# Optimization experiments

Hardware: AMD Instinct MI355X
Metric: run time of the kernel (lower is better)

Reference implementation:

```python
import jax, jax.numpy as jnp
import numpy as np
from jax import lax

C = 192       # filter_channels
L = 3         # n_layers
K = 3         # kernel_size
NB = 10       # num_bins
TB = 5.0      # tail_bound
HALF = 1      # in_channels // 2


def setup_inputs() -> dict:
    key = jax.random.key(0)
    ks = jax.random.split(key, 8)
    s = lambda i, shape: jax.random.normal(ks[i], shape, jnp.float32) * 0.05
    return {
        "x": jax.random.normal(ks[0], (16, 2, 8192), jnp.float32),
        "x_mask": jnp.ones((16, 1, 8192), jnp.float32),
        "w_pre": s(1, (C, HALF)), "b_pre": jnp.zeros((C,), jnp.float32),
        "sep_w": s(2, (L, K, 1, C)), "sep_b": jnp.zeros((L, C), jnp.float32),
        "pw_w": s(3, (L, C, C)), "pw_b": jnp.zeros((L, C), jnp.float32),
        "n1_g": jnp.ones((L, C), jnp.float32), "n1_b": jnp.zeros((L, C), jnp.float32),
        "n2_g": jnp.ones((L, C), jnp.float32), "n2_b": jnp.zeros((L, C), jnp.float32),
        "w_proj": s(4, (HALF * (3 * NB - 1), C)),
        "b_proj": jnp.zeros((HALF * (3 * NB - 1),), jnp.float32),
    }


def _layernorm_c(x, g, b, eps=1e-5):
    # normalize over channel axis (axis=1) of [b, c, t]
    m = jnp.mean(x, axis=1, keepdims=True)
    v = jnp.var(x, axis=1, keepdims=True)
    return (x - m) * lax.rsqrt(v + eps) * g[:, None] + b[:, None]


def _rq_spline(x, uw, uh, ud, tail_bound=TB, mw=1e-3, mh=1e-3, md=1e-3):
    """Unconstrained rational-quadratic spline with linear tails (forward)."""
    nb = uw.shape[-1]
    inside = (x >= -tail_bound) & (x <= tail_bound)
    const = float(np.log(np.exp(1.0 - md) - 1.0))
    ud = jnp.pad(ud, [(0, 0)] * (ud.ndim - 1) + [(1, 1)], constant_values=const)

    widths = jax.nn.softmax(uw, axis=-1)
    widths = mw + (1.0 - mw * nb) * widths
    cw = jnp.pad(jnp.cumsum(widths, -1), [(0, 0)] * (widths.ndim - 1) + [(1, 0)])
    cw = -tail_bound + 2.0 * tail_bound * cw
    cw = cw.at[..., 0].set(-tail_bound).at[..., -1].set(tail_bound)
    w = cw[..., 1:] - cw[..., :-1]

    heights = jax.nn.softmax(uh, axis=-1)
    heights = mh + (1.0 - mh * nb) * heights
    ch = jnp.pad(jnp.cumsum(heights, -1), [(0, 0)] * (heights.ndim - 1) + [(1, 0)])
    ch = -tail_bound + 2.0 * tail_bound * ch
    ch = ch.at[..., 0].set(-tail_bound).at[..., -1].set(tail_bound)
    hgt = ch[..., 1:] - ch[..., :-1]

    d = md + jax.nn.softplus(ud)  # [..., nb+1]

    xi = jnp.clip(x, -tail_bound, tail_bound)
    # searchsorted-style bin lookup
    idx = jnp.clip(jnp.sum((xi[..., None] >= cw).astype(jnp.int32), -1) - 1, 0, nb - 1)
    take = lambda p: jnp.take_along_axis(p, idx[..., None], axis=-1)[..., 0]

    in_cw, in_w = take(cw), take(w)
    in_ch, in_h = take(ch), take(hgt)
    in_d, d_p = take(d), take(d[..., 1:])
    delta = in_h / in_w

    th = (xi - in_cw) / in_w
    th1 = th * (1.0 - th)
    num = in_h * (delta * th * th + in_d * th1)
    den = delta + (in_d + d_p - 2.0 * delta) * th1
    y = in_ch + num / den
    dnum = delta * delta * (d_p * th * th + 2.0 * delta * th1 + in_d * (1.0 - th) ** 2)
    lad = jnp.log(dnum) - 2.0 * jnp.log(den)

    y = jnp.where(inside, y, x)
    lad = jnp.where(inside, lad, jnp.zeros_like(lad))
    return y, lad


def reference(x, x_mask, w_pre, b_pre, sep_w, sep_b, pw_w, pw_b,
              n1_g, n1_b, n2_g, n2_b, w_proj, b_proj):
    x0, x1 = x[:, :HALF], x[:, HALF:]

    # pre: 1x1 conv
    h = jnp.einsum('bct,fc->bft', x0, w_pre) + b_pre[:, None]

    # DDSConv: depthwise dilated conv + 1x1 + LayerNorm + GELU, residual
    for i in range(L):
        y = lax.conv_general_dilated(
            h * x_mask, sep_w[i], window_strides=(1,), padding='SAME',
            rhs_dilation=(K ** i,),
            dimension_numbers=('NCH', 'HIO', 'NCH'),
            feature_group_count=C) + sep_b[i][:, None]
        y = jax.nn.gelu(_layernorm_c(y, n1_g[i], n1_b[i]), approximate=False)
        y = jnp.einsum('bct,oc->bot', y, pw_w[i]) + pw_b[i][:, None]
        y = jax.nn.gelu(_layernorm_c(y, n2_g[i], n2_b[i]), approximate=False)
        h = h + y
    h = h * x_mask

    # proj: 1x1 conv to spline params
    h = (jnp.einsum('bct,oc->bot', h, w_proj) + b_proj[:, None]) * x_mask

    b, c, t = x0.shape
    h = h.reshape(b, c, 3 * NB - 1, t).transpose(0, 1, 3, 2)  # [b, c, t, 3*NB-1]
    scale = 1.0 / np.sqrt(C).astype(np.float32)
    uw = h[..., :NB] * scale
    uh = h[..., NB:2 * NB] * scale
    ud = h[..., 2 * NB:]

    y1, lad = _rq_spline(x1, uw, uh, ud)
    out = jnp.concatenate([x0, y1], axis=1) * x_mask
    logdet = jnp.sum(lad * x_mask, axis=(1, 2))
    return out, logdet
```

## Files before the change

### kernel.cpp

```cpp
#include <hip/hip_runtime.h>

#define CC    192
#define EXT   76
#define LDC   216
#define NTH   512
#define NW    8
#define HALO  13
#define INTR  50
#define TT    8192
#define BATCH 16
#define NTILES 164
#define NPROJ 29

#define WQ1_ELEMS (3*6*12*512)
#define WQ2_ELEMS (6*2*512)

typedef __bf16 bf16x8 __attribute__((ext_vector_type(8)));
typedef __bf16 bf16x4 __attribute__((ext_vector_type(4)));
typedef float  f32x4  __attribute__((ext_vector_type(4)));

__device__ __forceinline__ float gelu_fast(float v) {
    float vv = v * v;
    float u2 = v * fmaf(0.0713548162f, vv, 1.5957691216f);
    float t  = __expf(u2);
    float r  = __builtin_amdgcn_rcpf(t + 1.0f);
    return v - v * r;
}
__device__ __forceinline__ float softplus_f(float v) {
    float e = __expf(-fabsf(v));
    return fmaxf(v, 0.0f) + __logf(1.0f + e);
}

__global__ __launch_bounds__(256) void prepack_kernel(
    const float* __restrict__ pw_w, const float* __restrict__ w_proj,
    __bf16* __restrict__ wq, __bf16* __restrict__ wq2) {
    int idx = blockIdx.x * 256 + threadIdx.x;
    if (idx < WQ1_ELEMS) {
        int e    = idx & 7;
        int lane = (idx >> 3) & 63;
        int r    = idx >> 9;
        int mt   = r % 12;
        int ks   = (r / 12) % 6;
        int li   = r / 72;
        int o = 16 * mt + (lane & 15);
        int c = 32 * ks + 8 * (lane >> 4) + e;
        wq[idx] = (__bf16)pw_w[((size_t)li * CC + o) * CC + c];
    } else if (idx < WQ1_ELEMS + WQ2_ELEMS) {
        int i2   = idx - WQ1_ELEMS;
        int e    = i2 & 7;
        int lane = (i2 >> 3) & 63;
        int r    = i2 >> 9;
        int mt   = r % 2;
        int ks   = r / 2;
        int row  = 16 * mt + (lane & 15);
        int c    = 32 * ks + 8 * (lane >> 4) + e;
        wq2[i2] = (row < NPROJ) ? (__bf16)w_proj[(size_t)row * CC + c] : (__bf16)0.0f;
    }
}

__global__ __launch_bounds__(NTH, 4) void convflow_kernel(
    const float* __restrict__ x, const float* __restrict__ xmask,
    const float* __restrict__ w_pre, const float* __restrict__ b_pre,
    const float* __restrict__ sep_w, const float* __restrict__ sep_b,
    const __bf16* __restrict__ wq, const __bf16* __restrict__ wq2,
    const float* __restrict__ pw_b,
    const float* __restrict__ n1_g, const float* __restrict__ n1_b,
    const float* __restrict__ n2_g, const float* __restrict__ n2_b,
    const float* __restrict__ b_proj,
    float* __restrict__ out, float* __restrict__ logdet)
{
    extern __shared__ char smemraw[];
    __bf16* __restrict__ sh_t = (__bf16*)smemraw;
    __bf16* __restrict__ syt  = sh_t + 80 * LDC;
    float*  __restrict__ sproj = (float*)syt;
    float*  __restrict__ fbase = (float*)(syt + 80 * LDC);
    float*  __restrict__ spb = fbase;
    float*  __restrict__ sg2 = fbase + 192;
    float*  __restrict__ sb2 = fbase + 384;
    float*  __restrict__ sx0 = fbase + 576;
    float*  __restrict__ sx1 = fbase + 656;
    float*  __restrict__ smk = fbase + 736;

    const int tid  = threadIdx.x;
    const int lane = tid & 63;
    const int wav  = tid >> 6;
    const int b    = blockIdx.x / NTILES;
    const int tile = blockIdx.x - b * NTILES;
    const int t0   = tile * INTR - HALO;

    for (int j = tid; j < 80; j += NTH) {
        int t = t0 + j;
        bool ok = (j < EXT) && (t >= 0) && (t < TT);
        sx0[j] = ok ? x[b*2*TT + t]      : 0.0f;
        sx1[j] = ok ? x[b*2*TT + TT + t] : 0.0f;
        smk[j] = ok ? xmask[b*TT + t]    : 0.0f;
    }
    for (int e = tid; e < 80*LDC/2; e += NTH) ((float*)syt)[e] = 0.0f;
    for (int e = tid; e < 4*LDC/2;  e += NTH) ((float*)(sh_t + 76*LDC))[e] = 0.0f;
    __syncthreads();

    for (int e = tid; e < CC*EXT; e += NTH) {
        int c = e % CC;
        int j = e / CC;
        sh_t[j*LDC + c] = (__bf16)(sx0[j] * w_pre[c] + b_pre[c]);
    }
    for (int q = tid; q < INTR; q += NTH) {
        int t = t0 + HALO + q;
        if (t < TT) out[b*2*TT + t] = sx0[HALO+q] * smk[HALO+q];
    }
    __syncthreads();

    const int cA = lane, cB = lane + 64, cD = lane + 128;
    const int g   = lane >> 4;
    const int c15 = lane & 15;

    #pragma unroll
    for (int li = 0; li < 3; ++li) {
        constexpr int DILA[3] = {1, 3, 9};
        constexpr int JLOA[3] = {1, 4, 13};
        const int dil = DILA[li];
        const int jlo = JLOA[li], jhi = EXT - JLOA[li];

        for (int i = tid; i < CC; i += NTH) {
            spb[i] = pw_b[li*CC + i];
            sg2[i] = n2_g[li*CC + i];
            sb2[i] = n2_b[li*CC + i];
        }

        {
            float k0a = sep_w[(li*3+0)*CC + cA], k1a = sep_w[(li*3+1)*CC + cA], k2a = sep_w[(li*3+2)*CC + cA];
            float k0b = sep_w[(li*3+0)*CC + cB], k1b = sep_w[(li*3+1)*CC + cB], k2b = sep_w[(li*3+2)*CC + cB];
            float k0d = sep_w[(li*3+0)*CC + cD], k1d = sep_w[(li*3+1)*CC + cD], k2d = sep_w[(li*3+2)*CC + cD];
            float cba = sep_b[li*CC + cA], cbb = sep_b[li*CC + cB], cbd = sep_b[li*CC + cD];
            float g1a = n1_g[li*CC + cA], g1b = n1_g[li*CC + cB], g1d = n1_g[li*CC + cD];
            float b1a = n1_b[li*CC + cA], b1b = n1_b[li*CC + cB], b1d = n1_b[li*CC + cD];
            for (int j = jlo + wav; j < jhi; j += NW) {
                float m0 = smk[j-dil], m1 = smk[j], m2 = smk[j+dil];
                const __bf16* r0 = sh_t + (j-dil)*LDC;
                const __bf16* r1 = sh_t + j*LDC;
                const __bf16* r2 = sh_t + (j+dil)*LDC;
                float aa = k0a*(float)r0[cA]*m0 + k1a*(float)r1[cA]*m1 + k2a*(float)r2[cA]*m2 + cba;
                float ab = k0b*(float)r0[cB]*m0 + k1b*(float)r1[cB]*m1 + k2b*(float)r2[cB]*m2 + cbb;
                float ad = k0d*(float)r0[cD]*m0 + k1d*(float)r1[cD]*m1 + k2d*(float)r2[cD]*m2 + cbd;
                float s = aa+ab+ad, ss = aa*aa+ab*ab+ad*ad;
                #pragma unroll
                for (int mm = 1; mm < 64; mm <<= 1) { s += __shfl_xor(s, mm, 64); ss += __shfl_xor(ss, mm, 64); }
                float mean = s * (1.0f/CC);
                float var  = ss * (1.0f/CC) - mean*mean;
                float rstd = rsqrtf(var + 1e-5f);
                syt[j*LDC + cA] = (__bf16)gelu_fast((aa-mean)*rstd*g1a + b1a);
                syt[j*LDC + cB] = (__bf16)gelu_fast((ab-mean)*rstd*g1b + b1b);
                syt[j*LDC + cD] = (__bf16)gelu_fast((ad-mean)*rstd*g1d + b1d);
            }
        }
        __syncthreads();

        if (wav < 5) {
            const int nt = wav;
            f32x4 acc[12];
            #pragma unroll
            for (int mt = 0; mt < 12; ++mt) {
                float4 pb = *(const float4*)(spb + 16*mt + 4*g);
                acc[mt][0] = pb.x; acc[mt][1] = pb.y; acc[mt][2] = pb.z; acc[mt][3] = pb.w;
            }
            const __bf16* wql = wq + (size_t)li * (6*12*512);
            #pragma unroll
            for (int ks = 0; ks < 6; ++ks) {
                bf16x8 bfrag = *(const bf16x8*)(syt + (16*nt + c15)*LDC + 32*ks + 8*g);
                const __bf16* ap = wql + (size_t)(ks*12)*512 + lane*8;
                #pragma unroll
                for (int mt = 0; mt < 12; ++mt) {
                    bf16x8 afrag = *(const bf16x8*)(ap + (size_t)mt*512);
                    acc[mt] = __builtin_amdgcn_mfma_f32_16x16x32_bf16(afrag, bfrag, acc[mt], 0, 0, 0);
                }
            }
            float s = 0.0f, ss = 0.0f;
            #pragma unroll
            for (int mt = 0; mt < 12; ++mt) {
                #pragma unroll
                for (int e = 0; e < 4; ++e) { float z = acc[mt][e]; s += z; ss += z*z; }
            }
            s  += __shfl_xor(s, 16, 64);  s  += __shfl_xor(s, 32, 64);
            ss += __shfl_xor(ss, 16, 64); ss += __shfl_xor(ss, 32, 64);
            float mean = s * (1.0f/CC);
            float var  = ss * (1.0f/CC) - mean*mean;
            float rstd = rsqrtf(var + 1e-5f);
            const int col = 16*nt + c15;
            if (col < EXT) {
                #pragma unroll
                for (int mt = 0; mt < 12; ++mt) {
                    float4 gv = *(const float4*)(sg2 + 16*mt + 4*g);
                    float4 bv = *(const float4*)(sb2 + 16*mt + 4*g);
                    bf16x4 hv = *(bf16x4*)(sh_t + (size_t)col*LDC + 16*mt + 4*g);
                    float v0 = gelu_fast((acc[mt][0]-mean)*rstd*gv.x + bv.x);
                    float v1 = gelu_fast((acc[mt][1]-mean)*rstd*gv.y + bv.y);
                    float v2 = gelu_fast((acc[mt][2]-mean)*rstd*gv.z + bv.z);
                    float v3 = gelu_fast((acc[mt][3]-mean)*rstd*gv.w + bv.w);
                    hv[0] = (__bf16)((float)hv[0] + v0);
                    hv[1] = (__bf16)((float)hv[1] + v1);
                    hv[2] = (__bf16)((float)hv[2] + v2);
                    hv[3] = (__bf16)((float)hv[3] + v3);
                    *(bf16x4*)(sh_t + (size_t)col*LDC + 16*mt + 4*g) = hv;
                }
            }
        }
        __syncthreads();
    }

    if (wav < 5) {
        const int nt = wav;
        f32x4 p0 = {0,0,0,0}, p1 = {0,0,0,0};
        #pragma unroll
        for (int ks = 0; ks < 6; ++ks) {
            bf16x8 bfrag = *(const bf16x8*)(sh_t + (16*nt + c15)*LDC + 32*ks + 8*g);
            bf16x8 a0 = *(const bf16x8*)(wq2 + (size_t)(ks*2+0)*512 + lane*8);
            bf16x8 a1 = *(const bf16x8*)(wq2 + (size_t)(ks*2+1)*512 + lane*8);
            p0 = __builtin_amdgcn_mfma_f32_16x16x32_bf16(a0, bfrag, p0, 0, 0, 0);
            p1 = __builtin_amdgcn_mfma_f32_16x16x32_bf16(a1, bfrag, p1, 0, 0, 0);
        }
        const int col = 16*nt + c15;
        if (col >= HALO && col < HALO + INTR) {
            float mj = smk[col];
            #pragma unroll
            for (int e = 0; e < 4; ++e) {
                int p = 4*g + e;
                sproj[col*33 + p] = (p0[e]*mj + b_proj[p])*mj;
            }
            #pragma unroll
            for (int e = 0; e < 4; ++e) {
                int p = 16 + 4*g + e;
                if (p < NPROJ) sproj[col*33 + p] = (p1[e]*mj + b_proj[p])*mj;
            }
        }
    }
    __syncthreads();

    if (tid < 64) {
        int j = HALO + tid;
        int t = t0 + j;
        float ladm = 0.0f;
        if (tid < INTR && t < TT) {
            const float SCALE = 0.07216878364870323f;
            float mj = smk[j];
            float uw[10], uh[10];
            #pragma unroll
            for (int k = 0; k < 10; ++k) {
                uw[k] = sproj[j*33 + k]      * SCALE;
                uh[k] = sproj[j*33 + 10 + k] * SCALE;
            }
            float mxw = uw[0];
            #pragma unroll
            for (int k = 1; k < 10; ++k) mxw = fmaxf(mxw, uw[k]);
            float ew[10]; float sew = 0.0f;
            #pragma unroll
            for (int k = 0; k < 10; ++k) { ew[k] = __expf(uw[k]-mxw); sew += ew[k]; }
            float invw = 1.0f/sew;
            float cw[11]; cw[0] = -5.0f;
            float run = 0.0f;
            #pragma unroll
            for (int k = 0; k < 10; ++k) { run += 0.001f + 0.99f*ew[k]*invw; cw[k+1] = -5.0f + 10.0f*run; }
            cw[10] = 5.0f;
            float mxh = uh[0];
            #pragma unroll
            for (int k = 1; k < 10; ++k) mxh = fmaxf(mxh, uh[k]);
            float eh[10]; float seh = 0.0f;
            #pragma unroll
            for (int k = 0; k < 10; ++k) { eh[k] = __expf(uh[k]-mxh); seh += eh[k]; }
            float invh = 1.0f/seh;
            float ch[11]; ch[0] = -5.0f;
            run = 0.0f;
            #pragma unroll
            for (int k = 0; k < 10; ++k) { run += 0.001f + 0.99f*eh[k]*invh; ch[k+1] = -5.0f + 10.0f*run; }
            ch[10] = 5.0f;
            float dd[11];
            dd[0] = 1.0f;
            #pragma unroll
            for (int k = 0; k < 9; ++k) dd[k+1] = 0.001f + softplus_f(sproj[j*33 + 20 + k]);
            dd[10] = 1.0f;

            float xv = sx1[j];
            bool inside = (xv >= -5.0f) && (xv <= 5.0f);
            float xi = fminf(fmaxf(xv, -5.0f), 5.0f);
            int idx = 0;
            #pragma unroll
            for (int k = 1; k <= 9; ++k) idx = (xi >= cw[k]) ? k : idx;
            float in_cw=0, in_w=1, in_ch=0, in_h=1, in_d=1, d_p=1;
            #pragma unroll
            for (int k = 0; k < 10; ++k) {
                if (k == idx) {
                    in_cw = cw[k]; in_w = cw[k+1]-cw[k];
                    in_ch = ch[k]; in_h = ch[k+1]-ch[k];
                    in_d  = dd[k]; d_p  = dd[k+1];
                }
            }
            float delta = in_h/in_w;
            float th  = (xi - in_cw)/in_w;
            float th1 = th*(1.0f-th);
            float num = in_h*(delta*th*th + in_d*th1);
            float den = delta + (in_d + d_p - 2.0f*delta)*th1;
            float yv  = in_ch + num/den;
            float omt = 1.0f - th;
            float dnum = delta*delta*(d_p*th*th + 2.0f*delta*th1 + in_d*omt*omt);
            float lad = __logf(dnum) - 2.0f*__logf(den);
            if (!inside) { yv = xv; lad = 0.0f; }
            out[b*2*TT + TT + t] = yv*mj;
            ladm = lad*mj;
        }
        #pragma unroll
        for (int mm = 1; mm < 64; mm <<= 1) ladm += __shfl_xor(ladm, mm, 64);
        if (tid == 0) atomicAdd(&logdet[b], ladm);
    }
}

extern "C" void kernel_launch(void* const* d_in, const int* in_sizes, int n_in,
                              void* d_out, int out_size, void* d_ws, size_t ws_size,
                              hipStream_t stream) {
    const float* x      = (const float*)d_in[0];
    const float* xmask  = (const float*)d_in[1];
    const float* w_pre  = (const float*)d_in[2];
    const float* b_pre  = (const float*)d_in[3];
    const float* sep_w  = (const float*)d_in[4];
    const float* sep_b  = (const float*)d_in[5];
    const float* pw_w   = (const float*)d_in[6];
    const float* pw_b   = (const float*)d_in[7];
    const float* n1_g   = (const float*)d_in[8];
    const float* n1_b   = (const float*)d_in[9];
    const float* n2_g   = (const float*)d_in[10];
    const float* n2_b   = (const float*)d_in[11];
    const float* w_proj = (const float*)d_in[12];
    const float* b_proj = (const float*)d_in[13];
    float* out = (float*)d_out;
    float* logdet = out + (size_t)BATCH*2*TT;
    __bf16* wq  = (__bf16*)d_ws;
    __bf16* wq2 = wq + WQ1_ELEMS;

    hipMemsetAsync((void*)logdet, 0, BATCH*sizeof(float), stream);
    prepack_kernel<<<dim3((WQ1_ELEMS + WQ2_ELEMS + 255)/256), 256, 0, stream>>>(
        pw_w, w_proj, wq, wq2);

    size_t shbytes = (size_t)(2 * 80 * LDC * 2 + 816 * 4);
    dim3 grid(BATCH*NTILES);
    convflow_kernel<<<grid, NTH, shbytes, stream>>>(
        x, xmask, w_pre, b_pre, sep_w, sep_b, wq, wq2, pw_b,
        n1_g, n1_b, n2_g, n2_b, b_proj, out, logdet);
}
```

Baseline: 306.8 us.

## Shrink time tile to 64 columns and split MFMA output channels across all eight waves

Reduces the extended tile from 76 to 64 time steps (38 interior), so that 4 column tiles times 2 output-channel halves map onto all 8 waves instead of only 5. Each wave now computes 6 of 12 M-tiles, and the LayerNorm statistics are combined across the two halves through a small shared-memory reduction plus an extra barrier. The depthwise stage processes two rows per wave using 32-lane halves, and the zero-fill of shared buffers is dropped. The cost is more tiles, so more redundant halo recompute (13 of every 64 columns per side) and more blocks, traded for better wave utilisation and less shared memory per block.

After: 255.4 us. -16.8%, faster.

```diff
diff --git a/kernel.cpp b/kernel.cpp
--- a/kernel.cpp
+++ b/kernel.cpp
@@ -1,15 +1,15 @@
 #include <hip/hip_runtime.h>
 
 #define CC    192
-#define EXT   76
+#define EXT   64
 #define LDC   216
 #define NTH   512
 #define NW    8
 #define HALO  13
-#define INTR  50
+#define INTR  38
 #define TT    8192
 #define BATCH 16
-#define NTILES 164
+#define NTILES 216
 #define NPROJ 29
 
 #define WQ1_ELEMS (3*6*12*512)
@@ -50,9 +50,9 @@
         int e    = i2 & 7;
         int lane = (i2 >> 3) & 63;
         int r    = i2 >> 9;
-        int mt   = r % 2;
+        int pr   = r % 2;
         int ks   = r / 2;
-        int row  = 16 * mt + (lane & 15);
+        int row  = 16 * pr + (lane & 15);
         int c    = 32 * ks + 8 * (lane >> 4) + e;
         wq2[i2] = (row < NPROJ) ? (__bf16)w_proj[(size_t)row * CC + c] : (__bf16)0.0f;
     }
@@ -71,15 +71,16 @@
 {
     extern __shared__ char smemraw[];
     __bf16* __restrict__ sh_t = (__bf16*)smemraw;
-    __bf16* __restrict__ syt  = sh_t + 80 * LDC;
+    __bf16* __restrict__ syt  = sh_t + EXT * LDC;
     float*  __restrict__ sproj = (float*)syt;
-    float*  __restrict__ fbase = (float*)(syt + 80 * LDC);
+    float*  __restrict__ fbase = (float*)(syt + EXT * LDC);
     float*  __restrict__ spb = fbase;
     float*  __restrict__ sg2 = fbase + 192;
     float*  __restrict__ sb2 = fbase + 384;
     float*  __restrict__ sx0 = fbase + 576;
-    float*  __restrict__ sx1 = fbase + 656;
-    float*  __restrict__ smk = fbase + 736;
+    float*  __restrict__ sx1 = fbase + 640;
+    float*  __restrict__ smk = fbase + 704;
+    float2* __restrict__ sred = (float2*)(fbase + 768);
 
     const int tid  = threadIdx.x;
     const int lane = tid & 63;
@@ -88,15 +89,13 @@
     const int tile = blockIdx.x - b * NTILES;
     const int t0   = tile * INTR - HALO;
 
-    for (int j = tid; j < 80; j += NTH) {
+    for (int j = tid; j < EXT; j += NTH) {
         int t = t0 + j;
-        bool ok = (j < EXT) && (t >= 0) && (t < TT);
+        bool ok = (t >= 0) && (t < TT);
         sx0[j] = ok ? x[b*2*TT + t]      : 0.0f;
         sx1[j] = ok ? x[b*2*TT + TT + t] : 0.0f;
         smk[j] = ok ? xmask[b*TT + t]    : 0.0f;
     }
-    for (int e = tid; e < 80*LDC/2; e += NTH) ((float*)syt)[e] = 0.0f;
-    for (int e = tid; e < 4*LDC/2;  e += NTH) ((float*)(sh_t + 76*LDC))[e] = 0.0f;
     __syncthreads();
 
     for (int e = tid; e < CC*EXT; e += NTH) {
@@ -110,16 +109,20 @@
     }
     __syncthreads();
 
-    const int cA = lane, cB = lane + 64, cD = lane + 128;
     const int g   = lane >> 4;
     const int c15 = lane & 15;
+    const int cl  = lane & 31;
+    const int sub = lane >> 5;
+    const int nt   = wav & 3;
+    const int half = wav >> 2;
 
     #pragma unroll
     for (int li = 0; li < 3; ++li) {
         constexpr int DILA[3] = {1, 3, 9};
         constexpr int JLOA[3] = {1, 4, 13};
+        constexpr int JHIA[3] = {63, 60, 51};
         const int dil = DILA[li];
-        const int jlo = JLOA[li], jhi = EXT - JLOA[li];
+        const int jlo = JLOA[li], jhi = JHIA[li];
 
         for (int i = tid; i < CC; i += NTH) {
             spb[i] = pw_b[li*CC + i];
@@ -128,108 +131,110 @@
         }
 
         {
-            float k0a = sep_w[(li*3+0)*CC + cA], k1a = sep_w[(li*3+1)*CC + cA], k2a = sep_w[(li*3+2)*CC + cA];
-            float k0b = sep_w[(li*3+0)*CC + cB], k1b = sep_w[(li*3+1)*CC + cB], k2b = sep_w[(li*3+2)*CC + cB];
-            float k0d = sep_w[(li*3+0)*CC + cD], k1d = sep_w[(li*3+1)*CC + cD], k2d = sep_w[(li*3+2)*CC + cD];
-            float cba = sep_b[li*CC + cA], cbb = sep_b[li*CC + cB], cbd = sep_b[li*CC + cD];
-            float g1a = n1_g[li*CC + cA], g1b = n1_g[li*CC + cB], g1d = n1_g[li*CC + cD];
-            float b1a = n1_b[li*CC + cA], b1b = n1_b[li*CC + cB], b1d = n1_b[li*CC + cD];
-            for (int j = jlo + wav; j < jhi; j += NW) {
+            float k0[6], k1[6], k2[6], cb[6], g1[6], b1[6];
+            #pragma unroll
+            for (int k = 0; k < 6; ++k) {
+                int c = cl + 32*k;
+                k0[k] = sep_w[(li*3+0)*CC + c];
+                k1[k] = sep_w[(li*3+1)*CC + c];
+                k2[k] = sep_w[(li*3+2)*CC + c];
+                cb[k] = sep_b[li*CC + c];
+                g1[k] = n1_g[li*CC + c];
+                b1[k] = n1_b[li*CC + c];
+            }
+            for (int j = jlo + 2*wav + sub; j < jhi; j += 16) {
                 float m0 = smk[j-dil], m1 = smk[j], m2 = smk[j+dil];
                 const __bf16* r0 = sh_t + (j-dil)*LDC;
                 const __bf16* r1 = sh_t + j*LDC;
                 const __bf16* r2 = sh_t + (j+dil)*LDC;
-                float aa = k0a*(float)r0[cA]*m0 + k1a*(float)r1[cA]*m1 + k2a*(float)r2[cA]*m2 + cba;
-                float ab = k0b*(float)r0[cB]*m0 + k1b*(float)r1[cB]*m1 + k2b*(float)r2[cB]*m2 + cbb;
-                float ad = k0d*(float)r0[cD]*m0 + k1d*(float)r1[cD]*m1 + k2d*(float)r2[cD]*m2 + cbd;
-                float s = aa+ab+ad, ss = aa*aa+ab*ab+ad*ad;
-                #pragma unroll
-                for (int mm = 1; mm < 64; mm <<= 1) { s += __shfl_xor(s, mm, 64); ss += __shfl_xor(ss, mm, 64); }
+                float a[6]; float s = 0.0f, ss = 0.0f;
+                #pragma unroll
+                for (int k = 0; k < 6; ++k) {
+                    int c = cl + 32*k;
+                    float v = k0[k]*(float)r0[c]*m0 + k1[k]*(float)r1[c]*m1
+                            + k2[k]*(float)r2[c]*m2 + cb[k];
+                    a[k] = v; s += v; ss += v*v;
+                }
+                #pragma unroll
+                for (int mm = 1; mm < 32; mm <<= 1) {
+                    s  += __shfl_xor(s,  mm, 64);
+                    ss += __shfl_xor(ss, mm, 64);
+                }
                 float mean = s * (1.0f/CC);
                 float var  = ss * (1.0f/CC) - mean*mean;
                 float rstd = rsqrtf(var + 1e-5f);
-                syt[j*LDC + cA] = (__bf16)gelu_fast((aa-mean)*rstd*g1a + b1a);
-                syt[j*LDC + cB] = (__bf16)gelu_fast((ab-mean)*rstd*g1b + b1b);
-                syt[j*LDC + cD] = (__bf16)gelu_fast((ad-mean)*rstd*g1d + b1d);
+                #pragma unroll
+                for (int k = 0; k < 6; ++k)
+                    syt[j*LDC + cl + 32*k] = (__bf16)gelu_fast((a[k]-mean)*rstd*g1[k] + b1[k]);
             }
         }
         __syncthreads();
 
-        if (wav < 5) {
-            const int nt = wav;
-            f32x4 acc[12];
-            #pragma unroll
-            for (int mt = 0; mt < 12; ++mt) {
-                float4 pb = *(const float4*)(spb + 16*mt + 4*g);
-                acc[mt][0] = pb.x; acc[mt][1] = pb.y; acc[mt][2] = pb.z; acc[mt][3] = pb.w;
+        {
+            f32x4 acc[6];
+            #pragma unroll
+            for (int q = 0; q < 6; ++q) {
+                float4 pb = *(const float4*)(spb + 16*(6*half+q) + 4*g);
+                acc[q][0] = pb.x; acc[q][1] = pb.y; acc[q][2] = pb.z; acc[q][3] = pb.w;
             }
             const __bf16* wql = wq + (size_t)li * (6*12*512);
             #pragma unroll
             for (int ks = 0; ks < 6; ++ks) {
                 bf16x8 bfrag = *(const bf16x8*)(syt + (16*nt + c15)*LDC + 32*ks + 8*g);
-                const __bf16* ap = wql + (size_t)(ks*12)*512 + lane*8;
-                #pragma unroll
-                for (int mt = 0; mt < 12; ++mt) {
-                    bf16x8 afrag = *(const bf16x8*)(ap + (size_t)mt*512);
-                    acc[mt] = __builtin_amdgcn_mfma_f32_16x16x32_bf16(afrag, bfrag, acc[mt], 0, 0, 0);
+                const __bf16* ap = wql + (size_t)(ks*12 + 6*half)*512 + lane*8;
+                #pragma unroll
+                for (int q = 0; q < 6; ++q) {
+                    bf16x8 afrag = *(const bf16x8*)(ap + (size_t)q*512);
+                    acc[q] = __builtin_amdgcn_mfma_f32_16x16x32_bf16(afrag, bfrag, acc[q], 0, 0, 0);
                 }
             }
             float s = 0.0f, ss = 0.0f;
             #pragma unroll
-            for (int mt = 0; mt < 12; ++mt) {
-                #pragma unroll
-                for (int e = 0; e < 4; ++e) { float z = acc[mt][e]; s += z; ss += z*z; }
+            for (int q = 0; q < 6; ++q) {
+                #pragma unroll
+                for (int e = 0; e < 4; ++e) { float z = acc[q][e]; s += z; ss += z*z; }
             }
             s  += __shfl_xor(s, 16, 64);  s  += __shfl_xor(s, 32, 64);
             ss += __shfl_xor(ss, 16, 64); ss += __shfl_xor(ss, 32, 64);
-            float mean = s * (1.0f/CC);
-            float var  = ss * (1.0f/CC) - mean*mean;
+            if (lane < 16) sred[(16*nt + lane)*2 + half] = make_float2(s, ss);
+            __syncthreads();
+            const int col = 16*nt + c15;
+            float2 e0 = sred[col*2], e1 = sred[col*2+1];
+            float mean = (e0.x + e1.x) * (1.0f/CC);
+            float var  = (e0.y + e1.y) * (1.0f/CC) - mean*mean;
             float rstd = rsqrtf(var + 1e-5f);
-            const int col = 16*nt + c15;
-            if (col < EXT) {
-                #pragma unroll
-                for (int mt = 0; mt < 12; ++mt) {
-                    float4 gv = *(const float4*)(sg2 + 16*mt + 4*g);
-                    float4 bv = *(const float4*)(sb2 + 16*mt + 4*g);
-                    bf16x4 hv = *(bf16x4*)(sh_t + (size_t)col*LDC + 16*mt + 4*g);
-                    float v0 = gelu_fast((acc[mt][0]-mean)*rstd*gv.x + bv.x);
-                    float v1 = gelu_fast((acc[mt][1]-mean)*rstd*gv.y + bv.y);
-                    float v2 = gelu_fast((acc[mt][2]-mean)*rstd*gv.z + bv.z);
-                    float v3 = gelu_fast((acc[mt][3]-mean)*rstd*gv.w + bv.w);
-                    hv[0] = (__bf16)((float)hv[0] + v0);
-                    hv[1] = (__bf16)((float)hv[1] + v1);
-                    hv[2] = (__bf16)((float)hv[2] + v2);
-                    hv[3] = (__bf16)((float)hv[3] + v3);
-                    *(bf16x4*)(sh_t + (size_t)col*LDC + 16*mt + 4*g) = hv;
-                }
+            #pragma unroll
+            for (int q = 0; q < 6; ++q) {
+                int mt = 6*half + q;
+                float4 gv = *(const float4*)(sg2 + 16*mt + 4*g);
+                float4 bv = *(const float4*)(sb2 + 16*mt + 4*g);
+                bf16x4 hv = *(bf16x4*)(sh_t + (size_t)col*LDC + 16*mt + 4*g);
+                hv[0] = (__bf16)((float)hv[0] + gelu_fast((acc[q][0]-mean)*rstd*gv.x + bv.x));
+                hv[1] = (__bf16)((float)hv[1] + gelu_fast((acc[q][1]-mean)*rstd*gv.y + bv.y));
+                hv[2] = (__bf16)((float)hv[2] + gelu_fast((acc[q][2]-mean)*rstd*gv.z + bv.z));
+                hv[3] = (__bf16)((float)hv[3] + gelu_fast((acc[q][3]-mean)*rstd*gv.w + bv.w));
+                *(bf16x4*)(sh_t + (size_t)col*LDC + 16*mt + 4*g) = hv;
             }
         }
         __syncthreads();
     }
 
-    if (wav < 5) {
-        const int nt = wav;
-        f32x4 p0 = {0,0,0,0}, p1 = {0,0,0,0};
+    {
+        const int pr = half;
+        f32x4 p0 = {0,0,0,0};
         #pragma unroll
         for (int ks = 0; ks < 6; ++ks) {
             bf16x8 bfrag = *(const bf16x8*)(sh_t + (16*nt + c15)*LDC + 32*ks + 8*g);
-            bf16x8 a0 = *(const bf16x8*)(wq2 + (size_t)(ks*2+0)*512 + lane*8);
-            bf16x8 a1 = *(const bf16x8*)(wq2 + (size_t)(ks*2+1)*512 + lane*8);
+            bf16x8 a0 = *(const bf16x8*)(wq2 + (size_t)(ks*2 + pr)*512 + lane*8);
             p0 = __builtin_amdgcn_mfma_f32_16x16x32_bf16(a0, bfrag, p0, 0, 0, 0);
-            p1 = __builtin_amdgcn_mfma_f32_16x16x32_bf16(a1, bfrag, p1, 0, 0, 0);
         }
         const int col = 16*nt + c15;
         if (col >= HALO && col < HALO + INTR) {
             float mj = smk[col];
             #pragma unroll
             for (int e = 0; e < 4; ++e) {
-                int p = 4*g + e;
-                sproj[col*33 + p] = (p0[e]*mj + b_proj[p])*mj;
-            }
-            #pragma unroll
-            for (int e = 0; e < 4; ++e) {
-                int p = 16 + 4*g + e;
-                if (p < NPROJ) sproj[col*33 + p] = (p1[e]*mj + b_proj[p])*mj;
+                int p = 16*pr + 4*g + e;
+                if (p < NPROJ) sproj[col*33 + p] = (p0[e]*mj + b_proj[p])*mj;
             }
         }
     }
@@ -338,7 +343,7 @@
     prepack_kernel<<<dim3((WQ1_ELEMS + WQ2_ELEMS + 255)/256), 256, 0, stream>>>(
         pw_w, w_proj, wq, wq2);
 
-    size_t shbytes = (size_t)(2 * 80 * LDC * 2 + 816 * 4);
+    size_t shbytes = (size_t)(2*EXT*LDC*2 + 768*4 + 64*2*8);
     dim3 grid(BATCH*NTILES);
     convflow_kernel<<<grid, NTH, shbytes, stream>>>(
         x, xmask, w_pre, b_pre, sep_w, sep_b, wq, wq2, pw_b,
```
